# Kernel tuning notes

Hardware: AMD Instinct MI355X
Metric: run time of the kernel (lower is better)

The kernel has to match this reference:

```python
import jax, jax.numpy as jnp
import numpy as np

N_TOK = 2048      # flattened batch*seq tokens
D_MODEL = 1024    # in_features
D_INT = 512       # d_intermediate
N_EXPERTS = 8     # n_routed_experts
TOP_K = 2         # n_activated_experts


def setup_inputs() -> dict:
    key = jax.random.key(0)
    k1, k2, k3, k4, k5 = jax.random.split(key, 5)
    x = jax.random.normal(k1, (N_TOK, D_MODEL), dtype=jnp.float32)
    indices = jax.random.randint(k2, (N_TOK, TOP_K), 0, N_EXPERTS, dtype=jnp.int32)
    # router combine weights (normalized over top-k like a softmax router)
    weights = jax.nn.softmax(jax.random.normal(k3, (N_TOK, TOP_K), dtype=jnp.float32), axis=-1)
    # tokens-per-expert counts, consistent with indices (as the router would supply)
    counts = jnp.bincount(indices.reshape(-1), length=N_EXPERTS).astype(jnp.int32)
    # expert weights: fc1 -> 2*d_int (gated MLP), fc2 -> d_model; kaiming-ish scale
    s1 = 1.0 / np.sqrt(D_MODEL)
    s2 = 1.0 / np.sqrt(D_INT)
    fc1_weight = jax.random.uniform(k4, (N_EXPERTS, 2 * D_INT, D_MODEL), jnp.float32, -s1, s1)
    fc2_weight = jax.random.uniform(k5, (N_EXPERTS, D_MODEL, D_INT), jnp.float32, -s2, s2)
    return {"x": x, "weights": weights, "indices": indices, "counts": counts,
            "fc1_weight": fc1_weight, "fc2_weight": fc2_weight}


def reference(x, weights, indices, counts, fc1_weight, fc2_weight):
    # Dense dispatch-free formulation: run every token through every expert's
    # gated MLP, then gather the per-slot expert output. Identical math to the
    # sort / grouped-GEMM / scatter path for the selected (token, expert) pairs.
    # h: (n_tok, n_experts, 2*d_int)
    h = jnp.einsum('td,egd->teg', x, fc1_weight)
    y, z = jnp.split(h, 2, axis=-1)
    a = y * jax.nn.silu(z)  # GatedMLP: y * activation(z)
    # expert outputs: (n_tok, n_experts, d_model)
    out = jnp.einsum('tei,edi->ted', a, fc2_weight)
    # gather the chosen expert output for each of the top-k slots: (n_tok, k, d_model)
    per_slot = jnp.take_along_axis(out, indices[:, :, None], axis=1)
    # combine: z = bmm(weights[:, None], x_by_expert).squeeze(1)
    return jnp.einsum('tk,tkd->td', weights, per_slot)
```

## Files before the change

kernel.cpp:

```cpp
#include <hip/hip_runtime.h>

typedef unsigned short u16;
typedef unsigned int u32;
using short8  = __attribute__((ext_vector_type(8))) short;
using floatx4 = __attribute__((ext_vector_type(4))) float;

#define N_TOK   2048
#define D_MODEL 1024
#define D_INT   512
#define NE      8

#define O_TOK    0
#define O_WROW   24576
#define O_XG     65536
#define O_ACT    10551296
#define O_FC1B   36765696
#define O_FC2B   53542912

static __device__ inline u16 f2bf(float f) {
    u32 u = __builtin_bit_cast(u32, f);
    u = (u + 0x7fffu + ((u >> 16) & 1u)) >> 16;
    return (u16)u;
}
static __device__ inline u32 pack2(float a, float b) {
    return (u32)f2bf(a) | ((u32)f2bf(b) << 16);
}
static __device__ inline void glds16(const u16* g, u16* l) {
    __builtin_amdgcn_global_load_lds(
        (const __attribute__((address_space(1))) void*)g,
        (__attribute__((address_space(3))) void*)l, 16, 0, 0);
}

__global__ __launch_bounds__(256) void prep_kernel(
    const float* __restrict__ x, const float* __restrict__ wts,
    const int* __restrict__ indices, const int* __restrict__ counts,
    const float* __restrict__ fc1, const float* __restrict__ fc2,
    u16* __restrict__ fc1b, u16* __restrict__ fc2b,
    u16* __restrict__ Xg, int* __restrict__ tok, float* __restrict__ wrow,
    float* __restrict__ out) {
    int b = blockIdx.x, tid = threadIdx.x;
    if (b < 6144) {
        size_t v = (size_t)b * 256 + tid;
        const float* src; u16* dst; size_t off;
        if (v < 1048576) { src = fc1; dst = fc1b; off = v * 8; }
        else             { src = fc2; dst = fc2b; off = (v - 1048576) * 8; }
        const floatx4* s4 = reinterpret_cast<const floatx4*>(src + off);
        floatx4 a = s4[0], bb = s4[1];
        uint4 o;
        o.x = pack2(a[0], a[1]); o.y = pack2(a[2], a[3]);
        o.z = pack2(bb[0], bb[1]); o.w = pack2(bb[2], bb[3]);
        *reinterpret_cast<uint4*>(dst + off) = o;
        return;
    }
    if (b < 8192) {
        int t = b - 6144;
        int off[NE];
        {
            int acc = 0;
            #pragma unroll
            for (int e = 0; e < NE; e++) { off[e] = acc; acc += ((counts[e] + 63) >> 6) << 6; }
        }
        int e0 = indices[2 * t], e1 = indices[2 * t + 1];
        __shared__ int s0, s1;
        if (tid == 0) { s0 = 0; s1 = 0; }
        __syncthreads();
        int c0 = 0, c1 = 0;
        const int4* ip = reinterpret_cast<const int4*>(indices);
        #pragma unroll
        for (int i = 0; i < 4; i++) {
            int4 vv = ip[tid * 4 + i];
            int q = tid * 16 + i * 4;
            c0 += (q + 0 < 2 * t && vv.x == e0) + (q + 1 < 2 * t && vv.y == e0)
                + (q + 2 < 2 * t && vv.z == e0) + (q + 3 < 2 * t && vv.w == e0);
            c1 += (q + 0 <= 2 * t && vv.x == e1) + (q + 1 <= 2 * t && vv.y == e1)
                + (q + 2 <= 2 * t && vv.z == e1) + (q + 3 <= 2 * t && vv.w == e1);
        }
        if (c0) atomicAdd(&s0, c0);
        if (c1) atomicAdd(&s1, c1);
        __syncthreads();
        int r0 = off[e0] + s0;
        int r1 = off[e1] + s1;
        if (tid == 0) {
            tok[r0] = t; tok[r1] = t;
            wrow[r0] = wts[2 * t]; wrow[r1] = wts[2 * t + 1];
        }
        const floatx4* src = reinterpret_cast<const floatx4*>(x + (size_t)t * D_MODEL);
        floatx4 a = src[tid];
        uint2 o;
        o.x = pack2(a[0], a[1]); o.y = pack2(a[2], a[3]);
        *reinterpret_cast<uint2*>(Xg + (size_t)r0 * D_MODEL + tid * 4) = o;
        *reinterpret_cast<uint2*>(Xg + (size_t)r1 * D_MODEL + tid * 4) = o;
        return;
    }
    {
        int z = b - 8192;
        floatx4* dst = reinterpret_cast<floatx4*>(out) + (size_t)z * 1024;
        #pragma unroll
        for (int i = 0; i < 4; i++) dst[i * 256 + tid] = (floatx4){0.f, 0.f, 0.f, 0.f};
        return;
    }
}

__global__ __launch_bounds__(256) void gemm1_kernel(
    const u16* __restrict__ Xg, const u16* __restrict__ fc1b,
    u16* __restrict__ Act, const int* __restrict__ counts) {
    __shared__ u16 As[64 * 64];
    __shared__ u16 Bs[128 * 64];
    int tid = threadIdx.x;
    int soff[NE + 1];
    {
        int acc = 0;
        #pragma unroll
        for (int e2 = 0; e2 < NE; e2++) { soff[e2] = acc; acc += ((counts[e2] + 63) >> 6) << 6; }
        soff[NE] = acc;
    }
    int row0 = blockIdx.y * 64;
    if (row0 >= soff[NE]) return;
    int e = 0;
    while (soff[e + 1] <= row0) e++;
    int bx = blockIdx.x;
    const u16* A  = Xg + (size_t)row0 * 1024;
    const u16* Be = fc1b + (size_t)e * 1024 * 1024;

    int lane = tid & 63, w = tid >> 6;
    int m0 = (w >> 1) * 32, n0 = (w & 1) * 32;
    int lr = lane & 15, kq = lane >> 4;

    const u16* gA[2]; u16* lA[2];
    #pragma unroll
    for (int j = 0; j < 2; j++) {
        int v = tid + j * 256;
        int r = v >> 3, kb = (v & 7) ^ (r & 7);
        gA[j] = A + (size_t)r * 1024 + kb * 8;
        lA[j] = As + (w * 64 + j * 256) * 8;
    }
    const u16* gB[4]; u16* lB[4];
    #pragma unroll
    for (int j = 0; j < 4; j++) {
        int v = tid + j * 256;
        int r = v >> 3, kb = (v & 7) ^ (r & 7);
        int grow = (r < 64) ? (bx * 64 + r) : (448 + bx * 64 + r);
        gB[j] = Be + (size_t)grow * 1024 + kb * 8;
        lB[j] = Bs + (w * 64 + j * 256) * 8;
    }

    floatx4 aY[2][2], aZ[2][2];
    #pragma unroll
    for (int i = 0; i < 2; i++)
        #pragma unroll
        for (int j = 0; j < 2; j++) {
            aY[i][j] = (floatx4){0.f, 0.f, 0.f, 0.f};
            aZ[i][j] = (floatx4){0.f, 0.f, 0.f, 0.f};
        }

    for (int k0 = 0; k0 < 1024; k0 += 64) {
        glds16(gA[0] + k0, lA[0]); glds16(gA[1] + k0, lA[1]);
        glds16(gB[0] + k0, lB[0]); glds16(gB[1] + k0, lB[1]);
        glds16(gB[2] + k0, lB[2]); glds16(gB[3] + k0, lB[3]);
        __syncthreads();
        #pragma unroll
        for (int ks = 0; ks < 2; ks++) {
            int sw = ((ks * 4 + kq) ^ (lr & 7)) * 8;
            short8 af[2], by[2], bz[2];
            #pragma unroll
            for (int i = 0; i < 2; i++)
                af[i] = *reinterpret_cast<const short8*>(&As[(m0 + i * 16 + lr) * 64 + sw]);
            #pragma unroll
            for (int j = 0; j < 2; j++) {
                by[j] = *reinterpret_cast<const short8*>(&Bs[(n0 + j * 16 + lr) * 64 + sw]);
                bz[j] = *reinterpret_cast<const short8*>(&Bs[(64 + n0 + j * 16 + lr) * 64 + sw]);
            }
            #pragma unroll
            for (int i = 0; i < 2; i++)
                #pragma unroll
                for (int j = 0; j < 2; j++) {
                    aY[i][j] = __builtin_amdgcn_mfma_f32_16x16x32_bf16(af[i], by[j], aY[i][j], 0, 0, 0);
                    aZ[i][j] = __builtin_amdgcn_mfma_f32_16x16x32_bf16(af[i], bz[j], aZ[i][j], 0, 0, 0);
                }
        }
        __syncthreads();
    }
    #pragma unroll
    for (int i = 0; i < 2; i++)
        #pragma unroll
        for (int j = 0; j < 2; j++) {
            floatx4 y = aY[i][j], z = aZ[i][j];
            #pragma unroll
            for (int r = 0; r < 4; r++) {
                float zz = z[r];
                float av = y[r] * (zz / (1.0f + __expf(-zz)));
                int m = m0 + i * 16 + kq * 4 + r;
                int g = bx * 64 + n0 + j * 16 + lr;
                Act[(size_t)(row0 + m) * D_INT + g] = f2bf(av);
            }
        }
}

__global__ __launch_bounds__(256) void gemm2_kernel(
    const u16* __restrict__ Act, const u16* __restrict__ fc2b,
    float* __restrict__ out, const int* __restrict__ counts,
    const int* __restrict__ tok, const float* __restrict__ wrow) {
    __shared__ u16 As[64 * 64];
    __shared__ u16 Bs[128 * 64];
    __shared__ int sTok[64];
    __shared__ float sW[64];
    int tid = threadIdx.x;
    int soff[NE + 1];
    {
        int acc = 0;
        #pragma unroll
        for (int e2 = 0; e2 < NE; e2++) { soff[e2] = acc; acc += ((counts[e2] + 63) >> 6) << 6; }
        soff[NE] = acc;
    }
    int row0 = blockIdx.y * 64;
    if (row0 >= soff[NE]) return;
    int e = 0;
    while (soff[e + 1] <= row0) e++;
    int bx = blockIdx.x;
    const u16* A  = Act + (size_t)row0 * 512;
    const u16* Be = fc2b + (size_t)e * 1024 * 512;

    int lane = tid & 63, w = tid >> 6;
    int m0 = (w >> 1) * 32, n0 = (w & 1) * 64;
    int lr = lane & 15, kq = lane >> 4;

    const u16* gA[2]; u16* lA[2];
    #pragma unroll
    for (int j = 0; j < 2; j++) {
        int v = tid + j * 256;
        int r = v >> 3, kb = (v & 7) ^ (r & 7);
        gA[j] = A + (size_t)r * 512 + kb * 8;
        lA[j] = As + (w * 64 + j * 256) * 8;
    }
    const u16* gB[4]; u16* lB[4];
    #pragma unroll
    for (int j = 0; j < 4; j++) {
        int v = tid + j * 256;
        int r = v >> 3, kb = (v & 7) ^ (r & 7);
        gB[j] = Be + (size_t)(bx * 128 + r) * 512 + kb * 8;
        lB[j] = Bs + (w * 64 + j * 256) * 8;
    }

    floatx4 acc[2][4];
    #pragma unroll
    for (int i = 0; i < 2; i++)
        #pragma unroll
        for (int j = 0; j < 4; j++) acc[i][j] = (floatx4){0.f, 0.f, 0.f, 0.f};

    for (int k0 = 0; k0 < 512; k0 += 64) {
        glds16(gA[0] + k0, lA[0]); glds16(gA[1] + k0, lA[1]);
        glds16(gB[0] + k0, lB[0]); glds16(gB[1] + k0, lB[1]);
        glds16(gB[2] + k0, lB[2]); glds16(gB[3] + k0, lB[3]);
        __syncthreads();
        #pragma unroll
        for (int ks = 0; ks < 2; ks++) {
            int sw = ((ks * 4 + kq) ^ (lr & 7)) * 8;
            short8 af[2], bf[4];
            #pragma unroll
            for (int i = 0; i < 2; i++)
                af[i] = *reinterpret_cast<const short8*>(&As[(m0 + i * 16 + lr) * 64 + sw]);
            #pragma unroll
            for (int j = 0; j < 4; j++)
                bf[j] = *reinterpret_cast<const short8*>(&Bs[(n0 + j * 16 + lr) * 64 + sw]);
            #pragma unroll
            for (int i = 0; i < 2; i++)
                #pragma unroll
                for (int j = 0; j < 4; j++)
                    acc[i][j] = __builtin_amdgcn_mfma_f32_16x16x32_bf16(af[i], bf[j], acc[i][j], 0, 0, 0);
        }
        __syncthreads();
    }
    if (tid < 64) {
        int g = row0 + tid;
        bool val = (g - soff[e]) < counts[e];
        sTok[tid] = val ? tok[g] : -1;
        sW[tid]   = val ? wrow[g] : 0.f;
    }
    __syncthreads();
    #pragma unroll
    for (int i = 0; i < 2; i++)
        #pragma unroll
        for (int r = 0; r < 4; r++) {
            int m = m0 + i * 16 + kq * 4 + r;
            int t = sTok[m];
            if (t >= 0) {
                float wgt = sW[m];
                float* dst = out + (size_t)t * D_MODEL + bx * 128;
                #pragma unroll
                for (int j = 0; j < 4; j++)
                    atomicAdd(dst + n0 + j * 16 + lr, wgt * acc[i][j][r]);
            }
        }
}

extern "C" void kernel_launch(void* const* d_in, const int* in_sizes, int n_in,
                              void* d_out, int out_size, void* d_ws, size_t ws_size,
                              hipStream_t stream) {
    const float* x       = (const float*)d_in[0];
    const float* wts     = (const float*)d_in[1];
    const int*   indices = (const int*)d_in[2];
    const int*   counts  = (const int*)d_in[3];
    const float* fc1     = (const float*)d_in[4];
    const float* fc2     = (const float*)d_in[5];
    float* out = (float*)d_out;
    char* ws = (char*)d_ws;

    int*   tok  = (int*)(ws + O_TOK);
    float* wrow = (float*)(ws + O_WROW);
    u16*   Xg   = (u16*)(ws + O_XG);
    u16*   Act  = (u16*)(ws + O_ACT);
    u16*   fc1b = (u16*)(ws + O_FC1B);
    u16*   fc2b = (u16*)(ws + O_FC2B);

    prep_kernel<<<8704, 256, 0, stream>>>(x, wts, indices, counts, fc1, fc2,
                                          fc1b, fc2b, Xg, tok, wrow, out);
    gemm1_kernel<<<dim3(8, 72), 256, 0, stream>>>(Xg, fc1b, Act, counts);
    gemm2_kernel<<<dim3(8, 72), 256, 0, stream>>>(Act, fc2b, out, counts, tok, wrow);
}
```

Measured before the change: 151.6 us.

## Double-buffer LDS tiles in both expert GEMM kernels to overlap loads with MFMA

Both grouped GEMM kernels now keep two LDS buffers for the A and B tiles. The first tile is loaded before the loop, and each iteration issues the direct global-to-LDS loads for the next K tile before running MFMAs on the current one. This aims to hide global load latency behind compute and removes the barrier that followed the loads. In exchange LDS use per block doubles, which may lower occupancy, and correctness depends on the end-of-loop barrier waiting for the outstanding loads.

```diff
diff --git a/kernel.cpp b/kernel.cpp
--- a/kernel.cpp
+++ b/kernel.cpp
@@ -104,8 +104,8 @@
 __global__ __launch_bounds__(256) void gemm1_kernel(
     const u16* __restrict__ Xg, const u16* __restrict__ fc1b,
     u16* __restrict__ Act, const int* __restrict__ counts) {
-    __shared__ u16 As[64 * 64];
-    __shared__ u16 Bs[128 * 64];
+    __shared__ u16 As[2][64 * 64];
+    __shared__ u16 Bs[2][128 * 64];
     int tid = threadIdx.x;
     int soff[NE + 1];
     {
@@ -126,22 +126,22 @@
     int m0 = (w >> 1) * 32, n0 = (w & 1) * 32;
     int lr = lane & 15, kq = lane >> 4;
 
-    const u16* gA[2]; u16* lA[2];
+    const u16* gA[2]; int oA[2];
     #pragma unroll
     for (int j = 0; j < 2; j++) {
         int v = tid + j * 256;
         int r = v >> 3, kb = (v & 7) ^ (r & 7);
         gA[j] = A + (size_t)r * 1024 + kb * 8;
-        lA[j] = As + (w * 64 + j * 256) * 8;
-    }
-    const u16* gB[4]; u16* lB[4];
+        oA[j] = (w * 64 + j * 256) * 8;
+    }
+    const u16* gB[4]; int oB[4];
     #pragma unroll
     for (int j = 0; j < 4; j++) {
         int v = tid + j * 256;
         int r = v >> 3, kb = (v & 7) ^ (r & 7);
         int grow = (r < 64) ? (bx * 64 + r) : (448 + bx * 64 + r);
         gB[j] = Be + (size_t)grow * 1024 + kb * 8;
-        lB[j] = Bs + (w * 64 + j * 256) * 8;
+        oB[j] = (w * 64 + j * 256) * 8;
     }
 
     floatx4 aY[2][2], aZ[2][2];
@@ -153,22 +153,31 @@
             aZ[i][j] = (floatx4){0.f, 0.f, 0.f, 0.f};
         }
 
+    glds16(gA[0], &As[0][oA[0]]); glds16(gA[1], &As[0][oA[1]]);
+    glds16(gB[0], &Bs[0][oB[0]]); glds16(gB[1], &Bs[0][oB[1]]);
+    glds16(gB[2], &Bs[0][oB[2]]); glds16(gB[3], &Bs[0][oB[3]]);
+    __syncthreads();
+
     for (int k0 = 0; k0 < 1024; k0 += 64) {
-        glds16(gA[0] + k0, lA[0]); glds16(gA[1] + k0, lA[1]);
-        glds16(gB[0] + k0, lB[0]); glds16(gB[1] + k0, lB[1]);
-        glds16(gB[2] + k0, lB[2]); glds16(gB[3] + k0, lB[3]);
-        __syncthreads();
+        int buf = (k0 >> 6) & 1;
+        int nk = k0 + 64;
+        if (nk < 1024) {
+            int nb = buf ^ 1;
+            glds16(gA[0] + nk, &As[nb][oA[0]]); glds16(gA[1] + nk, &As[nb][oA[1]]);
+            glds16(gB[0] + nk, &Bs[nb][oB[0]]); glds16(gB[1] + nk, &Bs[nb][oB[1]]);
+            glds16(gB[2] + nk, &Bs[nb][oB[2]]); glds16(gB[3] + nk, &Bs[nb][oB[3]]);
+        }
         #pragma unroll
         for (int ks = 0; ks < 2; ks++) {
             int sw = ((ks * 4 + kq) ^ (lr & 7)) * 8;
             short8 af[2], by[2], bz[2];
             #pragma unroll
             for (int i = 0; i < 2; i++)
-                af[i] = *reinterpret_cast<const short8*>(&As[(m0 + i * 16 + lr) * 64 + sw]);
+                af[i] = *reinterpret_cast<const short8*>(&As[buf][(m0 + i * 16 + lr) * 64 + sw]);
             #pragma unroll
             for (int j = 0; j < 2; j++) {
-                by[j] = *reinterpret_cast<const short8*>(&Bs[(n0 + j * 16 + lr) * 64 + sw]);
-                bz[j] = *reinterpret_cast<const short8*>(&Bs[(64 + n0 + j * 16 + lr) * 64 + sw]);
+                by[j] = *reinterpret_cast<const short8*>(&Bs[buf][(n0 + j * 16 + lr) * 64 + sw]);
+                bz[j] = *reinterpret_cast<const short8*>(&Bs[buf][(64 + n0 + j * 16 + lr) * 64 + sw]);
             }
             #pragma unroll
             for (int i = 0; i < 2; i++)
@@ -200,8 +209,8 @@
     const u16* __restrict__ Act, const u16* __restrict__ fc2b,
     float* __restrict__ out, const int* __restrict__ counts,
     const int* __restrict__ tok, const float* __restrict__ wrow) {
-    __shared__ u16 As[64 * 64];
-    __shared__ u16 Bs[128 * 64];
+    __shared__ u16 As[2][64 * 64];
+    __shared__ u16 Bs[2][128 * 64];
     __shared__ int sTok[64];
     __shared__ float sW[64];
     int tid = threadIdx.x;
@@ -224,21 +233,21 @@
     int m0 = (w >> 1) * 32, n0 = (w & 1) * 64;
     int lr = lane & 15, kq = lane >> 4;
 
-    const u16* gA[2]; u16* lA[2];
+    const u16* gA[2]; int oA[2];
     #pragma unroll
     for (int j = 0; j < 2; j++) {
         int v = tid + j * 256;
         int r = v >> 3, kb = (v & 7) ^ (r & 7);
         gA[j] = A + (size_t)r * 512 + kb * 8;
-        lA[j] = As + (w * 64 + j * 256) * 8;
-    }
-    const u16* gB[4]; u16* lB[4];
+        oA[j] = (w * 64 + j * 256) * 8;
+    }
+    const u16* gB[4]; int oB[4];
     #pragma unroll
     for (int j = 0; j < 4; j++) {
         int v = tid + j * 256;
         int r = v >> 3, kb = (v & 7) ^ (r & 7);
         gB[j] = Be + (size_t)(bx * 128 + r) * 512 + kb * 8;
-        lB[j] = Bs + (w * 64 + j * 256) * 8;
+        oB[j] = (w * 64 + j * 256) * 8;
     }
 
     floatx4 acc[2][4];
@@ -247,21 +256,30 @@
         #pragma unroll
         for (int j = 0; j < 4; j++) acc[i][j] = (floatx4){0.f, 0.f, 0.f, 0.f};
 
+    glds16(gA[0], &As[0][oA[0]]); glds16(gA[1], &As[0][oA[1]]);
+    glds16(gB[0], &Bs[0][oB[0]]); glds16(gB[1], &Bs[0][oB[1]]);
+    glds16(gB[2], &Bs[0][oB[2]]); glds16(gB[3], &Bs[0][oB[3]]);
+    __syncthreads();
+
     for (int k0 = 0; k0 < 512; k0 += 64) {
-        glds16(gA[0] + k0, lA[0]); glds16(gA[1] + k0, lA[1]);
-        glds16(gB[0] + k0, lB[0]); glds16(gB[1] + k0, lB[1]);
-        glds16(gB[2] + k0, lB[2]); glds16(gB[3] + k0, lB[3]);
-        __syncthreads();
+        int buf = (k0 >> 6) & 1;
+        int nk = k0 + 64;
+        if (nk < 512) {
+            int nb = buf ^ 1;
+            glds16(gA[0] + nk, &As[nb][oA[0]]); glds16(gA[1] + nk, &As[nb][oA[1]]);
+            glds16(gB[0] + nk, &Bs[nb][oB[0]]); glds16(gB[1] + nk, &Bs[nb][oB[1]]);
+            glds16(gB[2] + nk, &Bs[nb][oB[2]]); glds16(gB[3] + nk, &Bs[nb][oB[3]]);
+        }
         #pragma unroll
         for (int ks = 0; ks < 2; ks++) {
             int sw = ((ks * 4 + kq) ^ (lr & 7)) * 8;
             short8 af[2], bf[4];
             #pragma unroll
             for (int i = 0; i < 2; i++)
-                af[i] = *reinterpret_cast<const short8*>(&As[(m0 + i * 16 + lr) * 64 + sw]);
+                af[i] = *reinterpret_cast<const short8*>(&As[buf][(m0 + i * 16 + lr) * 64 + sw]);
             #pragma unroll
             for (int j = 0; j < 4; j++)
-                bf[j] = *reinterpret_cast<const short8*>(&Bs[(n0 + j * 16 + lr) * 64 + sw]);
+                bf[j] = *reinterpret_cast<const short8*>(&Bs[buf][(n0 + j * 16 + lr) * 64 + sw]);
             #pragma unroll
             for (int i = 0; i < 2; i++)
                 #pragma unroll
```

New measurement: 153.7 us. No clear change (+1.4%).

## Fuse fp32-to-bf16 conversion and token gather into the grouped GEMM loads

Applied to the files above, without the earlier changes.

Drops the prep pass that converted all expert weights and gathered x rows into bf16 workspace buffers. The GEMMs now read fp32 x (gathered via the token table) and fp32 fc1/fc2 directly, convert to bf16 in registers and store into LDS. The routing kernel shrinks to computing the token/weight tables and zeroing the output. This removes a large standalone read/write pass over the weights. In exchange each GEMM block reads twice the bytes per tile, repeats the conversion across row blocks, and gives up the direct global-to-LDS loads for those operands.

```diff
diff --git a/kernel.cpp b/kernel.cpp
--- a/kernel.cpp
+++ b/kernel.cpp
@@ -11,11 +11,8 @@
 #define NE      8
 
 #define O_TOK    0
-#define O_WROW   24576
-#define O_XG     65536
-#define O_ACT    10551296
-#define O_FC1B   36765696
-#define O_FC2B   53542912
+#define O_WROW   32768
+#define O_ACT    65536
 
 static __device__ inline u16 f2bf(float f) {
     u32 u = __builtin_bit_cast(u32, f);
@@ -25,85 +22,67 @@
 static __device__ inline u32 pack2(float a, float b) {
     return (u32)f2bf(a) | ((u32)f2bf(b) << 16);
 }
+static __device__ inline uint4 pack8(floatx4 a, floatx4 b) {
+    uint4 o;
+    o.x = pack2(a[0], a[1]); o.y = pack2(a[2], a[3]);
+    o.z = pack2(b[0], b[1]); o.w = pack2(b[2], b[3]);
+    return o;
+}
 static __device__ inline void glds16(const u16* g, u16* l) {
     __builtin_amdgcn_global_load_lds(
         (const __attribute__((address_space(1))) void*)g,
         (__attribute__((address_space(3))) void*)l, 16, 0, 0);
 }
 
-__global__ __launch_bounds__(256) void prep_kernel(
-    const float* __restrict__ x, const float* __restrict__ wts,
-    const int* __restrict__ indices, const int* __restrict__ counts,
-    const float* __restrict__ fc1, const float* __restrict__ fc2,
-    u16* __restrict__ fc1b, u16* __restrict__ fc2b,
-    u16* __restrict__ Xg, int* __restrict__ tok, float* __restrict__ wrow,
-    float* __restrict__ out) {
+__global__ __launch_bounds__(256) void route_kernel(
+    const float* __restrict__ wts, const int* __restrict__ indices,
+    const int* __restrict__ counts,
+    int* __restrict__ tok, float* __restrict__ wrow, float* __restrict__ out) {
     int b = blockIdx.x, tid = threadIdx.x;
-    if (b < 6144) {
-        size_t v = (size_t)b * 256 + tid;
-        const float* src; u16* dst; size_t off;
-        if (v < 1048576) { src = fc1; dst = fc1b; off = v * 8; }
-        else             { src = fc2; dst = fc2b; off = (v - 1048576) * 8; }
-        const floatx4* s4 = reinterpret_cast<const floatx4*>(src + off);
-        floatx4 a = s4[0], bb = s4[1];
-        uint4 o;
-        o.x = pack2(a[0], a[1]); o.y = pack2(a[2], a[3]);
-        o.z = pack2(bb[0], bb[1]); o.w = pack2(bb[2], bb[3]);
-        *reinterpret_cast<uint4*>(dst + off) = o;
+    if (b >= 2048) {
+        int z = b - 2048;
+        floatx4* dst = reinterpret_cast<floatx4*>(out) + (size_t)z * 1024;
+        #pragma unroll
+        for (int i = 0; i < 4; i++) dst[i * 256 + tid] = (floatx4){0.f, 0.f, 0.f, 0.f};
         return;
     }
-    if (b < 8192) {
-        int t = b - 6144;
-        int off[NE];
-        {
-            int acc = 0;
-            #pragma unroll
-            for (int e = 0; e < NE; e++) { off[e] = acc; acc += ((counts[e] + 63) >> 6) << 6; }
-        }
-        int e0 = indices[2 * t], e1 = indices[2 * t + 1];
-        __shared__ int s0, s1;
-        if (tid == 0) { s0 = 0; s1 = 0; }
-        __syncthreads();
-        int c0 = 0, c1 = 0;
-        const int4* ip = reinterpret_cast<const int4*>(indices);
-        #pragma unroll
-        for (int i = 0; i < 4; i++) {
-            int4 vv = ip[tid * 4 + i];
-            int q = tid * 16 + i * 4;
-            c0 += (q + 0 < 2 * t && vv.x == e0) + (q + 1 < 2 * t && vv.y == e0)
-                + (q + 2 < 2 * t && vv.z == e0) + (q + 3 < 2 * t && vv.w == e0);
-            c1 += (q + 0 <= 2 * t && vv.x == e1) + (q + 1 <= 2 * t && vv.y == e1)
-                + (q + 2 <= 2 * t && vv.z == e1) + (q + 3 <= 2 * t && vv.w == e1);
-        }
-        if (c0) atomicAdd(&s0, c0);
-        if (c1) atomicAdd(&s1, c1);
-        __syncthreads();
+    int t = b;
+    int off[NE];
+    {
+        int acc = 0;
+        #pragma unroll
+        for (int e = 0; e < NE; e++) { off[e] = acc; acc += ((counts[e] + 63) >> 6) << 6; }
+    }
+    int e0 = indices[2 * t], e1 = indices[2 * t + 1];
+    __shared__ int s0, s1;
+    if (tid == 0) { s0 = 0; s1 = 0; }
+    __syncthreads();
+    int c0 = 0, c1 = 0;
+    const int4* ip = reinterpret_cast<const int4*>(indices);
+    #pragma unroll
+    for (int i = 0; i < 4; i++) {
+        int4 vv = ip[tid * 4 + i];
+        int q = tid * 16 + i * 4;
+        c0 += (q + 0 < 2 * t && vv.x == e0) + (q + 1 < 2 * t && vv.y == e0)
+            + (q + 2 < 2 * t && vv.z == e0) + (q + 3 < 2 * t && vv.w == e0);
+        c1 += (q + 0 <= 2 * t && vv.x == e1) + (q + 1 <= 2 * t && vv.y == e1)
+            + (q + 2 <= 2 * t && vv.z == e1) + (q + 3 <= 2 * t && vv.w == e1);
+    }
+    if (c0) atomicAdd(&s0, c0);
+    if (c1) atomicAdd(&s1, c1);
+    __syncthreads();
+    if (tid == 0) {
         int r0 = off[e0] + s0;
         int r1 = off[e1] + s1;
-        if (tid == 0) {
-            tok[r0] = t; tok[r1] = t;
-            wrow[r0] = wts[2 * t]; wrow[r1] = wts[2 * t + 1];
-        }
-        const floatx4* src = reinterpret_cast<const floatx4*>(x + (size_t)t * D_MODEL);
-        floatx4 a = src[tid];
-        uint2 o;
-        o.x = pack2(a[0], a[1]); o.y = pack2(a[2], a[3]);
-        *reinterpret_cast<uint2*>(Xg + (size_t)r0 * D_MODEL + tid * 4) = o;
-        *reinterpret_cast<uint2*>(Xg + (size_t)r1 * D_MODEL + tid * 4) = o;
-        return;
-    }
-    {
-        int z = b - 8192;
-        floatx4* dst = reinterpret_cast<floatx4*>(out) + (size_t)z * 1024;
-        #pragma unroll
-        for (int i = 0; i < 4; i++) dst[i * 256 + tid] = (floatx4){0.f, 0.f, 0.f, 0.f};
-        return;
+        tok[r0] = t; tok[r1] = t;
+        wrow[r0] = wts[2 * t]; wrow[r1] = wts[2 * t + 1];
     }
 }
 
 __global__ __launch_bounds__(256) void gemm1_kernel(
-    const u16* __restrict__ Xg, const u16* __restrict__ fc1b,
-    u16* __restrict__ Act, const int* __restrict__ counts) {
+    const float* __restrict__ x, const float* __restrict__ fc1,
+    u16* __restrict__ Act, const int* __restrict__ counts,
+    const int* __restrict__ tok) {
     __shared__ u16 As[64 * 64];
     __shared__ u16 Bs[128 * 64];
     int tid = threadIdx.x;
@@ -118,30 +97,27 @@
     if (row0 >= soff[NE]) return;
     int e = 0;
     while (soff[e + 1] <= row0) e++;
+    int cnte = counts[e];
     int bx = blockIdx.x;
-    const u16* A  = Xg + (size_t)row0 * 1024;
-    const u16* Be = fc1b + (size_t)e * 1024 * 1024;
+    const float* Be = fc1 + (size_t)e * 1024 * 1024;
 
     int lane = tid & 63, w = tid >> 6;
     int m0 = (w >> 1) * 32, n0 = (w & 1) * 32;
     int lr = lane & 15, kq = lane >> 4;
 
-    const u16* gA[2]; u16* lA[2];
-    #pragma unroll
-    for (int j = 0; j < 2; j++) {
-        int v = tid + j * 256;
-        int r = v >> 3, kb = (v & 7) ^ (r & 7);
-        gA[j] = A + (size_t)r * 1024 + kb * 8;
-        lA[j] = As + (w * 64 + j * 256) * 8;
-    }
-    const u16* gB[4]; u16* lB[4];
+    int rA0 = tid >> 3, rA1 = rA0 + 32;
+    int kbA0 = (tid & 7) ^ (rA0 & 7), kbA1 = (tid & 7) ^ (rA1 & 7);
+    int tA0 = (row0 + rA0 - soff[e]) < cnte ? tok[row0 + rA0] : 0;
+    int tA1 = (row0 + rA1 - soff[e]) < cnte ? tok[row0 + rA1] : 0;
+    const float* gA0 = x + (size_t)tA0 * 1024 + kbA0 * 8;
+    const float* gA1 = x + (size_t)tA1 * 1024 + kbA1 * 8;
+    const float* gB[4];
     #pragma unroll
     for (int j = 0; j < 4; j++) {
         int v = tid + j * 256;
         int r = v >> 3, kb = (v & 7) ^ (r & 7);
         int grow = (r < 64) ? (bx * 64 + r) : (448 + bx * 64 + r);
         gB[j] = Be + (size_t)grow * 1024 + kb * 8;
-        lB[j] = Bs + (w * 64 + j * 256) * 8;
     }
 
     floatx4 aY[2][2], aZ[2][2];
@@ -154,9 +130,22 @@
         }
 
     for (int k0 = 0; k0 < 1024; k0 += 64) {
-        glds16(gA[0] + k0, lA[0]); glds16(gA[1] + k0, lA[1]);
-        glds16(gB[0] + k0, lB[0]); glds16(gB[1] + k0, lB[1]);
-        glds16(gB[2] + k0, lB[2]); glds16(gB[3] + k0, lB[3]);
+        floatx4 a0l = *reinterpret_cast<const floatx4*>(gA0 + k0);
+        floatx4 a0h = *reinterpret_cast<const floatx4*>(gA0 + k0 + 4);
+        floatx4 a1l = *reinterpret_cast<const floatx4*>(gA1 + k0);
+        floatx4 a1h = *reinterpret_cast<const floatx4*>(gA1 + k0 + 4);
+        floatx4 bl[4], bh[4];
+        #pragma unroll
+        for (int j = 0; j < 4; j++) {
+            bl[j] = *reinterpret_cast<const floatx4*>(gB[j] + k0);
+            bh[j] = *reinterpret_cast<const floatx4*>(gB[j] + k0 + 4);
+        }
+        __syncthreads();
+        *reinterpret_cast<uint4*>(&As[(size_t)tid * 8])         = pack8(a0l, a0h);
+        *reinterpret_cast<uint4*>(&As[(size_t)(tid + 256) * 8]) = pack8(a1l, a1h);
+        #pragma unroll
+        for (int j = 0; j < 4; j++)
+            *reinterpret_cast<uint4*>(&Bs[(size_t)(tid + j * 256) * 8]) = pack8(bl[j], bh[j]);
         __syncthreads();
         #pragma unroll
         for (int ks = 0; ks < 2; ks++) {
@@ -178,7 +167,6 @@
                     aZ[i][j] = __builtin_amdgcn_mfma_f32_16x16x32_bf16(af[i], bz[j], aZ[i][j], 0, 0, 0);
                 }
         }
-        __syncthreads();
     }
     #pragma unroll
     for (int i = 0; i < 2; i++)
@@ -197,7 +185,7 @@
 }
 
 __global__ __launch_bounds__(256) void gemm2_kernel(
-    const u16* __restrict__ Act, const u16* __restrict__ fc2b,
+    const u16* __restrict__ Act, const float* __restrict__ fc2,
     float* __restrict__ out, const int* __restrict__ counts,
     const int* __restrict__ tok, const float* __restrict__ wrow) {
     __shared__ u16 As[64 * 64];
@@ -218,27 +206,26 @@
     while (soff[e + 1] <= row0) e++;
     int bx = blockIdx.x;
     const u16* A  = Act + (size_t)row0 * 512;
-    const u16* Be = fc2b + (size_t)e * 1024 * 512;
+    const float* Be = fc2 + (size_t)e * 1024 * 512;
 
     int lane = tid & 63, w = tid >> 6;
     int m0 = (w >> 1) * 32, n0 = (w & 1) * 64;
     int lr = lane & 15, kq = lane >> 4;
 
-    const u16* gA[2]; u16* lA[2];
+    const u16* gA[2]; int oA[2];
     #pragma unroll
     for (int j = 0; j < 2; j++) {
         int v = tid + j * 256;
         int r = v >> 3, kb = (v & 7) ^ (r & 7);
         gA[j] = A + (size_t)r * 512 + kb * 8;
-        lA[j] = As + (w * 64 + j * 256) * 8;
-    }
-    const u16* gB[4]; u16* lB[4];
+        oA[j] = (w * 64 + j * 256) * 8;
+    }
+    const float* gB[4];
     #pragma unroll
     for (int j = 0; j < 4; j++) {
         int v = tid + j * 256;
         int r = v >> 3, kb = (v & 7) ^ (r & 7);
         gB[j] = Be + (size_t)(bx * 128 + r) * 512 + kb * 8;
-        lB[j] = Bs + (w * 64 + j * 256) * 8;
     }
 
     floatx4 acc[2][4];
@@ -248,9 +235,18 @@
         for (int j = 0; j < 4; j++) acc[i][j] = (floatx4){0.f, 0.f, 0.f, 0.f};
 
     for (int k0 = 0; k0 < 512; k0 += 64) {
-        glds16(gA[0] + k0, lA[0]); glds16(gA[1] + k0, lA[1]);
-        glds16(gB[0] + k0, lB[0]); glds16(gB[1] + k0, lB[1]);
-        glds16(gB[2] + k0, lB[2]); glds16(gB[3] + k0, lB[3]);
+        floatx4 bl[4], bh[4];
+        #pragma unroll
+        for (int j = 0; j < 4; j++) {
+            bl[j] = *reinterpret_cast<const floatx4*>(gB[j] + k0);
+            bh[j] = *reinterpret_cast<const floatx4*>(gB[j] + k0 + 4);
+        }
+        __syncthreads();
+        glds16(gA[0] + k0, &As[oA[0]]);
+        glds16(gA[1] + k0, &As[oA[1]]);
+        #pragma unroll
+        for (int j = 0; j < 4; j++)
+            *reinterpret_cast<uint4*>(&Bs[(size_t)(tid + j * 256) * 8]) = pack8(bl[j], bh[j]);
         __syncthreads();
         #pragma unroll
         for (int ks = 0; ks < 2; ks++) {
@@ -268,7 +264,6 @@
                 for (int j = 0; j < 4; j++)
                     acc[i][j] = __builtin_amdgcn_mfma_f32_16x16x32_bf16(af[i], bf[j], acc[i][j], 0, 0, 0);
         }
-        __syncthreads();
     }
     if (tid < 64) {
         int g = row0 + tid;
@@ -307,13 +302,9 @@
 
     int*   tok  = (int*)(ws + O_TOK);
     float* wrow = (float*)(ws + O_WROW);
-    u16*   Xg   = (u16*)(ws + O_XG);
     u16*   Act  = (u16*)(ws + O_ACT);
-    u16*   fc1b = (u16*)(ws + O_FC1B);
-    u16*   fc2b = (u16*)(ws + O_FC2B);
-
-    prep_kernel<<<8704, 256, 0, stream>>>(x, wts, indices, counts, fc1, fc2,
-                                          fc1b, fc2b, Xg, tok, wrow, out);
-    gemm1_kernel<<<dim3(8, 72), 256, 0, stream>>>(Xg, fc1b, Act, counts);
-    gemm2_kernel<<<dim3(8, 72), 256, 0, stream>>>(Act, fc2b, out, counts, tok, wrow);
-}
+
+    route_kernel<<<2560, 256, 0, stream>>>(wts, indices, counts, tok, wrow, out);
+    gemm1_kernel<<<dim3(8, 72), 256, 0, stream>>>(x, fc1, Act, counts, tok);
+    gemm2_kernel<<<dim3(8, 72), 256, 0, stream>>>(Act, fc2, out, counts, tok, wrow);
+}
```

Measured after the change: 164.5 us. 1.09x slower.

## Fuse prep and both expert GEMMs into one persistent cooperative kernel

Applied to the files above, without the earlier changes.

Merges the prep, gemm1 and gemm2 launches into a single persistent cooperative kernel of 512 blocks. Each block loops over the former block indices, and grid-wide syncs separate the three phases. This removes two kernel-launch gaps and the tail idle time between kernels. In exchange it adds grid barrier cost and limits parallelism to 512 resident blocks, so the prep phase with 8704 work items runs serially in strided loops.

```diff
diff --git a/kernel.cpp b/kernel.cpp
--- a/kernel.cpp
+++ b/kernel.cpp
@@ -1,4 +1,7 @@
 #include <hip/hip_runtime.h>
+#include <hip/hip_cooperative_groups.h>
+
+namespace cg = cooperative_groups;
 
 typedef unsigned short u16;
 typedef unsigned int u32;
@@ -31,266 +34,256 @@
         (__attribute__((address_space(3))) void*)l, 16, 0, 0);
 }
 
-__global__ __launch_bounds__(256) void prep_kernel(
+__global__ __launch_bounds__(256, 4) void moe_kernel(
     const float* __restrict__ x, const float* __restrict__ wts,
     const int* __restrict__ indices, const int* __restrict__ counts,
     const float* __restrict__ fc1, const float* __restrict__ fc2,
     u16* __restrict__ fc1b, u16* __restrict__ fc2b,
-    u16* __restrict__ Xg, int* __restrict__ tok, float* __restrict__ wrow,
+    u16* __restrict__ Xg, u16* __restrict__ Act,
+    int* __restrict__ tok, float* __restrict__ wrow,
     float* __restrict__ out) {
-    int b = blockIdx.x, tid = threadIdx.x;
-    if (b < 6144) {
-        size_t v = (size_t)b * 256 + tid;
-        const float* src; u16* dst; size_t off;
-        if (v < 1048576) { src = fc1; dst = fc1b; off = v * 8; }
-        else             { src = fc2; dst = fc2b; off = (v - 1048576) * 8; }
-        const floatx4* s4 = reinterpret_cast<const floatx4*>(src + off);
-        floatx4 a = s4[0], bb = s4[1];
-        uint4 o;
-        o.x = pack2(a[0], a[1]); o.y = pack2(a[2], a[3]);
-        o.z = pack2(bb[0], bb[1]); o.w = pack2(bb[2], bb[3]);
-        *reinterpret_cast<uint4*>(dst + off) = o;
-        return;
-    }
-    if (b < 8192) {
-        int t = b - 6144;
-        int off[NE];
-        {
-            int acc = 0;
-            #pragma unroll
-            for (int e = 0; e < NE; e++) { off[e] = acc; acc += ((counts[e] + 63) >> 6) << 6; }
-        }
-        int e0 = indices[2 * t], e1 = indices[2 * t + 1];
-        __shared__ int s0, s1;
-        if (tid == 0) { s0 = 0; s1 = 0; }
-        __syncthreads();
-        int c0 = 0, c1 = 0;
-        const int4* ip = reinterpret_cast<const int4*>(indices);
-        #pragma unroll
-        for (int i = 0; i < 4; i++) {
-            int4 vv = ip[tid * 4 + i];
-            int q = tid * 16 + i * 4;
-            c0 += (q + 0 < 2 * t && vv.x == e0) + (q + 1 < 2 * t && vv.y == e0)
-                + (q + 2 < 2 * t && vv.z == e0) + (q + 3 < 2 * t && vv.w == e0);
-            c1 += (q + 0 <= 2 * t && vv.x == e1) + (q + 1 <= 2 * t && vv.y == e1)
-                + (q + 2 <= 2 * t && vv.z == e1) + (q + 3 <= 2 * t && vv.w == e1);
-        }
-        if (c0) atomicAdd(&s0, c0);
-        if (c1) atomicAdd(&s1, c1);
-        __syncthreads();
-        int r0 = off[e0] + s0;
-        int r1 = off[e1] + s1;
-        if (tid == 0) {
-            tok[r0] = t; tok[r1] = t;
-            wrow[r0] = wts[2 * t]; wrow[r1] = wts[2 * t + 1];
-        }
-        const floatx4* src = reinterpret_cast<const floatx4*>(x + (size_t)t * D_MODEL);
-        floatx4 a = src[tid];
-        uint2 o;
-        o.x = pack2(a[0], a[1]); o.y = pack2(a[2], a[3]);
-        *reinterpret_cast<uint2*>(Xg + (size_t)r0 * D_MODEL + tid * 4) = o;
-        *reinterpret_cast<uint2*>(Xg + (size_t)r1 * D_MODEL + tid * 4) = o;
-        return;
-    }
-    {
-        int z = b - 8192;
-        floatx4* dst = reinterpret_cast<floatx4*>(out) + (size_t)z * 1024;
-        #pragma unroll
-        for (int i = 0; i < 4; i++) dst[i * 256 + tid] = (floatx4){0.f, 0.f, 0.f, 0.f};
-        return;
-    }
-}
-
-__global__ __launch_bounds__(256) void gemm1_kernel(
-    const u16* __restrict__ Xg, const u16* __restrict__ fc1b,
-    u16* __restrict__ Act, const int* __restrict__ counts) {
     __shared__ u16 As[64 * 64];
     __shared__ u16 Bs[128 * 64];
-    int tid = threadIdx.x;
+    __shared__ int sTok[64];
+    __shared__ float sW[64];
+    __shared__ int sCnt[2];
+
+    const int b = blockIdx.x, tid = threadIdx.x;
+    cg::grid_group grid = cg::this_grid();
+
     int soff[NE + 1];
     {
         int acc = 0;
         #pragma unroll
-        for (int e2 = 0; e2 < NE; e2++) { soff[e2] = acc; acc += ((counts[e2] + 63) >> 6) << 6; }
+        for (int e = 0; e < NE; e++) { soff[e] = acc; acc += ((counts[e] + 63) >> 6) << 6; }
         soff[NE] = acc;
     }
-    int row0 = blockIdx.y * 64;
-    if (row0 >= soff[NE]) return;
-    int e = 0;
-    while (soff[e + 1] <= row0) e++;
-    int bx = blockIdx.x;
-    const u16* A  = Xg + (size_t)row0 * 1024;
-    const u16* Be = fc1b + (size_t)e * 1024 * 1024;
-
-    int lane = tid & 63, w = tid >> 6;
-    int m0 = (w >> 1) * 32, n0 = (w & 1) * 32;
-    int lr = lane & 15, kq = lane >> 4;
-
-    const u16* gA[2]; u16* lA[2];
-    #pragma unroll
-    for (int j = 0; j < 2; j++) {
-        int v = tid + j * 256;
-        int r = v >> 3, kb = (v & 7) ^ (r & 7);
-        gA[j] = A + (size_t)r * 1024 + kb * 8;
-        lA[j] = As + (w * 64 + j * 256) * 8;
+    const int nT = (soff[NE] >> 6) * 8;
+
+    const int lane = tid & 63, w = tid >> 6;
+    const int lr = lane & 15, kq = lane >> 4;
+
+    #pragma unroll 1
+    for (int i = 0; i < 17; i++) {
+        int j = i * 512 + b;
+        if (j < 6144) {
+            size_t v = (size_t)j * 256 + tid;
+            const float* src; u16* dst; size_t off;
+            if (v < 1048576) { src = fc1; dst = fc1b; off = v * 8; }
+            else             { src = fc2; dst = fc2b; off = (v - 1048576) * 8; }
+            const floatx4* s4 = reinterpret_cast<const floatx4*>(src + off);
+            floatx4 a = s4[0], bb = s4[1];
+            uint4 o;
+            o.x = pack2(a[0], a[1]); o.y = pack2(a[2], a[3]);
+            o.z = pack2(bb[0], bb[1]); o.w = pack2(bb[2], bb[3]);
+            *reinterpret_cast<uint4*>(dst + off) = o;
+        } else if (j < 8192) {
+            int t = j - 6144;
+            int e0 = indices[2 * t], e1 = indices[2 * t + 1];
+            if (tid == 0) { sCnt[0] = 0; sCnt[1] = 0; }
+            __syncthreads();
+            int c0 = 0, c1 = 0;
+            const int4* ip = reinterpret_cast<const int4*>(indices);
+            #pragma unroll
+            for (int q4 = 0; q4 < 4; q4++) {
+                int4 vv = ip[tid * 4 + q4];
+                int q = tid * 16 + q4 * 4;
+                c0 += (q + 0 < 2 * t && vv.x == e0) + (q + 1 < 2 * t && vv.y == e0)
+                    + (q + 2 < 2 * t && vv.z == e0) + (q + 3 < 2 * t && vv.w == e0);
+                c1 += (q + 0 <= 2 * t && vv.x == e1) + (q + 1 <= 2 * t && vv.y == e1)
+                    + (q + 2 <= 2 * t && vv.z == e1) + (q + 3 <= 2 * t && vv.w == e1);
+            }
+            if (c0) atomicAdd(&sCnt[0], c0);
+            if (c1) atomicAdd(&sCnt[1], c1);
+            __syncthreads();
+            int r0 = soff[e0] + sCnt[0];
+            int r1 = soff[e1] + sCnt[1];
+            if (tid == 0) {
+                tok[r0] = t; tok[r1] = t;
+                wrow[r0] = wts[2 * t]; wrow[r1] = wts[2 * t + 1];
+            }
+            const floatx4* src = reinterpret_cast<const floatx4*>(x + (size_t)t * D_MODEL);
+            floatx4 a = src[tid];
+            uint2 o;
+            o.x = pack2(a[0], a[1]); o.y = pack2(a[2], a[3]);
+            *reinterpret_cast<uint2*>(Xg + (size_t)r0 * D_MODEL + tid * 4) = o;
+            *reinterpret_cast<uint2*>(Xg + (size_t)r1 * D_MODEL + tid * 4) = o;
+            __syncthreads();
+        } else {
+            int z = j - 8192;
+            floatx4* dst = reinterpret_cast<floatx4*>(out) + (size_t)z * 1024;
+            #pragma unroll
+            for (int q = 0; q < 4; q++) dst[q * 256 + tid] = (floatx4){0.f, 0.f, 0.f, 0.f};
+        }
     }
-    const u16* gB[4]; u16* lB[4];
-    #pragma unroll
-    for (int j = 0; j < 4; j++) {
-        int v = tid + j * 256;
-        int r = v >> 3, kb = (v & 7) ^ (r & 7);
-        int grow = (r < 64) ? (bx * 64 + r) : (448 + bx * 64 + r);
-        gB[j] = Be + (size_t)grow * 1024 + kb * 8;
-        lB[j] = Bs + (w * 64 + j * 256) * 8;
+    __threadfence();
+    grid.sync();
+
+    {
+        const int m0 = (w >> 1) * 32, n0 = (w & 1) * 32;
+        #pragma unroll 1
+        for (int T = b; T < nT; T += 512) {
+            int bx = T & 7, row0 = (T >> 3) * 64;
+            int e = 0;
+            while (soff[e + 1] <= row0) e++;
+            const u16* A  = Xg + (size_t)row0 * 1024;
+            const u16* Be = fc1b + (size_t)e * 1024 * 1024;
+
+            const u16* gA[2]; u16* lA[2];
+            #pragma unroll
+            for (int p = 0; p < 2; p++) {
+                int v = tid + p * 256;
+                int r = v >> 3, kb = (v & 7) ^ (r & 7);
+                gA[p] = A + (size_t)r * 1024 + kb * 8;
+                lA[p] = As + (size_t)(w * 64 + p * 256) * 8;
+            }
+            const u16* gB[4]; u16* lB[4];
+            #pragma unroll
+            for (int p = 0; p < 4; p++) {
+                int v = tid + p * 256;
+                int r = v >> 3, kb = (v & 7) ^ (r & 7);
+                int grow = (r < 64) ? (bx * 64 + r) : (448 + bx * 64 + r);
+                gB[p] = Be + (size_t)grow * 1024 + kb * 8;
+                lB[p] = Bs + (size_t)(w * 64 + p * 256) * 8;
+            }
+
+            floatx4 aY[2][2], aZ[2][2];
+            #pragma unroll
+            for (int i = 0; i < 2; i++)
+                #pragma unroll
+                for (int j = 0; j < 2; j++) {
+                    aY[i][j] = (floatx4){0.f, 0.f, 0.f, 0.f};
+                    aZ[i][j] = (floatx4){0.f, 0.f, 0.f, 0.f};
+                }
+
+            #pragma unroll 1
+            for (int k0 = 0; k0 < 1024; k0 += 64) {
+                glds16(gA[0] + k0, lA[0]); glds16(gA[1] + k0, lA[1]);
+                glds16(gB[0] + k0, lB[0]); glds16(gB[1] + k0, lB[1]);
+                glds16(gB[2] + k0, lB[2]); glds16(gB[3] + k0, lB[3]);
+                __syncthreads();
+                #pragma unroll
+                for (int ks = 0; ks < 2; ks++) {
+                    int sw = ((ks * 4 + kq) ^ (lr & 7)) * 8;
+                    short8 af[2], by[2], bz[2];
+                    #pragma unroll
+                    for (int i = 0; i < 2; i++)
+                        af[i] = *reinterpret_cast<const short8*>(&As[(m0 + i * 16 + lr) * 64 + sw]);
+                    #pragma unroll
+                    for (int j = 0; j < 2; j++) {
+                        by[j] = *reinterpret_cast<const short8*>(&Bs[(n0 + j * 16 + lr) * 64 + sw]);
+                        bz[j] = *reinterpret_cast<const short8*>(&Bs[(64 + n0 + j * 16 + lr) * 64 + sw]);
+                    }
+                    #pragma unroll
+                    for (int i = 0; i < 2; i++)
+                        #pragma unroll
+                        for (int j = 0; j < 2; j++) {
+                            aY[i][j] = __builtin_amdgcn_mfma_f32_16x16x32_bf16(af[i], by[j], aY[i][j], 0, 0, 0);
+                            aZ[i][j] = __builtin_amdgcn_mfma_f32_16x16x32_bf16(af[i], bz[j], aZ[i][j], 0, 0, 0);
+                        }
+                }
+                __syncthreads();
+            }
+            #pragma unroll
+            for (int i = 0; i < 2; i++)
+                #pragma unroll
+                for (int j = 0; j < 2; j++) {
+                    floatx4 y = aY[i][j], z = aZ[i][j];
+                    #pragma unroll
+                    for (int r = 0; r < 4; r++) {
+                        float zz = z[r];
+                        float av = y[r] * (zz / (1.0f + __expf(-zz)));
+                        int m = m0 + i * 16 + kq * 4 + r;
+                        int g = bx * 64 + n0 + j * 16 + lr;
+                        Act[(size_t)(row0 + m) * D_INT + g] = f2bf(av);
+                    }
+                }
+        }
     }
-
-    floatx4 aY[2][2], aZ[2][2];
-    #pragma unroll
-    for (int i = 0; i < 2; i++)
-        #pragma unroll
-        for (int j = 0; j < 2; j++) {
-            aY[i][j] = (floatx4){0.f, 0.f, 0.f, 0.f};
-            aZ[i][j] = (floatx4){0.f, 0.f, 0.f, 0.f};
+    __threadfence();
+    grid.sync();
+
+    {
+        const int m0 = (w >> 1) * 32, n0 = (w & 1) * 64;
+        #pragma unroll 1
+        for (int T = b; T < nT; T += 512) {
+            int bx = T & 7, row0 = (T >> 3) * 64;
+            int e = 0;
+            while (soff[e + 1] <= row0) e++;
+            const u16* A  = Act + (size_t)row0 * 512;
+            const u16* Be = fc2b + (size_t)e * 1024 * 512;
+
+            const u16* gA[2]; u16* lA[2];
+            #pragma unroll
+            for (int p = 0; p < 2; p++) {
+                int v = tid + p * 256;
+                int r = v >> 3, kb = (v & 7) ^ (r & 7);
+                gA[p] = A + (size_t)r * 512 + kb * 8;
+                lA[p] = As + (size_t)(w * 64 + p * 256) * 8;
+            }
+            const u16* gB[4]; u16* lB[4];
+            #pragma unroll
+            for (int p = 0; p < 4; p++) {
+                int v = tid + p * 256;
+                int r = v >> 3, kb = (v & 7) ^ (r & 7);
+                gB[p] = Be + (size_t)(bx * 128 + r) * 512 + kb * 8;
+                lB[p] = Bs + (size_t)(w * 64 + p * 256) * 8;
+            }
+
+            floatx4 acc[2][4];
+            #pragma unroll
+            for (int i = 0; i < 2; i++)
+                #pragma unroll
+                for (int j = 0; j < 4; j++) acc[i][j] = (floatx4){0.f, 0.f, 0.f, 0.f};
+
+            #pragma unroll 1
+            for (int k0 = 0; k0 < 512; k0 += 64) {
+                glds16(gA[0] + k0, lA[0]); glds16(gA[1] + k0, lA[1]);
+                glds16(gB[0] + k0, lB[0]); glds16(gB[1] + k0, lB[1]);
+                glds16(gB[2] + k0, lB[2]); glds16(gB[3] + k0, lB[3]);
+                __syncthreads();
+                #pragma unroll
+                for (int ks = 0; ks < 2; ks++) {
+                    int sw = ((ks * 4 + kq) ^ (lr & 7)) * 8;
+                    short8 af[2], bf[4];
+                    #pragma unroll
+                    for (int i = 0; i < 2; i++)
+                        af[i] = *reinterpret_cast<const short8*>(&As[(m0 + i * 16 + lr) * 64 + sw]);
+                    #pragma unroll
+                    for (int j = 0; j < 4; j++)
+                        bf[j] = *reinterpret_cast<const short8*>(&Bs[(n0 + j * 16 + lr) * 64 + sw]);
+                    #pragma unroll
+                    for (int i = 0; i < 2; i++)
+                        #pragma unroll
+                        for (int j = 0; j < 4; j++)
+                            acc[i][j] = __builtin_amdgcn_mfma_f32_16x16x32_bf16(af[i], bf[j], acc[i][j], 0, 0, 0);
+                }
+                __syncthreads();
+            }
+            if (tid < 64) {
+                int g = row0 + tid;
+                bool val = (g - soff[e]) < counts[e];
+                sTok[tid] = val ? tok[g] : -1;
+                sW[tid]   = val ? wrow[g] : 0.f;
+            }
+            __syncthreads();
+            #pragma unroll
+            for (int i = 0; i < 2; i++)
+                #pragma unroll
+                for (int r = 0; r < 4; r++) {
+                    int m = m0 + i * 16 + kq * 4 + r;
+                    int t = sTok[m];
+                    if (t >= 0) {
+                        float wgt = sW[m];
+                        float* dst = out + (size_t)t * D_MODEL + bx * 128;
+                        #pragma unroll
+                        for (int j = 0; j < 4; j++)
+                            atomicAdd(dst + n0 + j * 16 + lr, wgt * acc[i][j][r]);
+                    }
+                }
+            __syncthreads();
         }
-
-    for (int k0 = 0; k0 < 1024; k0 += 64) {
-        glds16(gA[0] + k0, lA[0]); glds16(gA[1] + k0, lA[1]);
-        glds16(gB[0] + k0, lB[0]); glds16(gB[1] + k0, lB[1]);
-        glds16(gB[2] + k0, lB[2]); glds16(gB[3] + k0, lB[3]);
-        __syncthreads();
-        #pragma unroll
-        for (int ks = 0; ks < 2; ks++) {
-            int sw = ((ks * 4 + kq) ^ (lr & 7)) * 8;
-            short8 af[2], by[2], bz[2];
-            #pragma unroll
-            for (int i = 0; i < 2; i++)
-                af[i] = *reinterpret_cast<const short8*>(&As[(m0 + i * 16 + lr) * 64 + sw]);
-            #pragma unroll
-            for (int j = 0; j < 2; j++) {
-                by[j] = *reinterpret_cast<const short8*>(&Bs[(n0 + j * 16 + lr) * 64 + sw]);
-                bz[j] = *reinterpret_cast<const short8*>(&Bs[(64 + n0 + j * 16 + lr) * 64 + sw]);
-            }
-            #pragma unroll
-            for (int i = 0; i < 2; i++)
-                #pragma unroll
-                for (int j = 0; j < 2; j++) {
-                    aY[i][j] = __builtin_amdgcn_mfma_f32_16x16x32_bf16(af[i], by[j], aY[i][j], 0, 0, 0);
-                    aZ[i][j] = __builtin_amdgcn_mfma_f32_16x16x32_bf16(af[i], bz[j], aZ[i][j], 0, 0, 0);
-                }
-        }
-        __syncthreads();
     }
-    #pragma unroll
-    for (int i = 0; i < 2; i++)
-        #pragma unroll
-        for (int j = 0; j < 2; j++) {
-            floatx4 y = aY[i][j], z = aZ[i][j];
-            #pragma unroll
-            for (int r = 0; r < 4; r++) {
-                float zz = z[r];
-                float av = y[r] * (zz / (1.0f + __expf(-zz)));
-                int m = m0 + i * 16 + kq * 4 + r;
-                int g = bx * 64 + n0 + j * 16 + lr;
-                Act[(size_t)(row0 + m) * D_INT + g] = f2bf(av);
-            }
-        }
-}
-
-__global__ __launch_bounds__(256) void gemm2_kernel(
-    const u16* __restrict__ Act, const u16* __restrict__ fc2b,
-    float* __restrict__ out, const int* __restrict__ counts,
-    const int* __restrict__ tok, const float* __restrict__ wrow) {
-    __shared__ u16 As[64 * 64];
-    __shared__ u16 Bs[128 * 64];
-    __shared__ int sTok[64];
-    __shared__ float sW[64];
-    int tid = threadIdx.x;
-    int soff[NE + 1];
-    {
-        int acc = 0;
-        #pragma unroll
-        for (int e2 = 0; e2 < NE; e2++) { soff[e2] = acc; acc += ((counts[e2] + 63) >> 6) << 6; }
-        soff[NE] = acc;
-    }
-    int row0 = blockIdx.y * 64;
-    if (row0 >= soff[NE]) return;
-    int e = 0;
-    while (soff[e + 1] <= row0) e++;
-    int bx = blockIdx.x;
-    const u16* A  = Act + (size_t)row0 * 512;
-    const u16* Be = fc2b + (size_t)e * 1024 * 512;
-
-    int lane = tid & 63, w = tid >> 6;
-    int m0 = (w >> 1) * 32, n0 = (w & 1) * 64;
-    int lr = lane & 15, kq = lane >> 4;
-
-    const u16* gA[2]; u16* lA[2];
-    #pragma unroll
-    for (int j = 0; j < 2; j++) {
-        int v = tid + j * 256;
-        int r = v >> 3, kb = (v & 7) ^ (r & 7);
-        gA[j] = A + (size_t)r * 512 + kb * 8;
-        lA[j] = As + (w * 64 + j * 256) * 8;
-    }
-    const u16* gB[4]; u16* lB[4];
-    #pragma unroll
-    for (int j = 0; j < 4; j++) {
-        int v = tid + j * 256;
-        int r = v >> 3, kb = (v & 7) ^ (r & 7);
-        gB[j] = Be + (size_t)(bx * 128 + r) * 512 + kb * 8;
-        lB[j] = Bs + (w * 64 + j * 256) * 8;
-    }
-
-    floatx4 acc[2][4];
-    #pragma unroll
-    for (int i = 0; i < 2; i++)
-        #pragma unroll
-        for (int j = 0; j < 4; j++) acc[i][j] = (floatx4){0.f, 0.f, 0.f, 0.f};
-
-    for (int k0 = 0; k0 < 512; k0 += 64) {
-        glds16(gA[0] + k0, lA[0]); glds16(gA[1] + k0, lA[1]);
-        glds16(gB[0] + k0, lB[0]); glds16(gB[1] + k0, lB[1]);
-        glds16(gB[2] + k0, lB[2]); glds16(gB[3] + k0, lB[3]);
-        __syncthreads();
-        #pragma unroll
-        for (int ks = 0; ks < 2; ks++) {
-            int sw = ((ks * 4 + kq) ^ (lr & 7)) * 8;
-            short8 af[2], bf[4];
-            #pragma unroll
-            for (int i = 0; i < 2; i++)
-                af[i] = *reinterpret_cast<const short8*>(&As[(m0 + i * 16 + lr) * 64 + sw]);
-            #pragma unroll
-            for (int j = 0; j < 4; j++)
-                bf[j] = *reinterpret_cast<const short8*>(&Bs[(n0 + j * 16 + lr) * 64 + sw]);
-            #pragma unroll
-            for (int i = 0; i < 2; i++)
-                #pragma unroll
-                for (int j = 0; j < 4; j++)
-                    acc[i][j] = __builtin_amdgcn_mfma_f32_16x16x32_bf16(af[i], bf[j], acc[i][j], 0, 0, 0);
-        }
-        __syncthreads();
-    }
-    if (tid < 64) {
-        int g = row0 + tid;
-        bool val = (g - soff[e]) < counts[e];
-        sTok[tid] = val ? tok[g] : -1;
-        sW[tid]   = val ? wrow[g] : 0.f;
-    }
-    __syncthreads();
-    #pragma unroll
-    for (int i = 0; i < 2; i++)
-        #pragma unroll
-        for (int r = 0; r < 4; r++) {
-            int m = m0 + i * 16 + kq * 4 + r;
-            int t = sTok[m];
-            if (t >= 0) {
-                float wgt = sW[m];
-                float* dst = out + (size_t)t * D_MODEL + bx * 128;
-                #pragma unroll
-                for (int j = 0; j < 4; j++)
-                    atomicAdd(dst + n0 + j * 16 + lr, wgt * acc[i][j][r]);
-            }
-        }
 }
 
 extern "C" void kernel_launch(void* const* d_in, const int* in_sizes, int n_in,
@@ -312,8 +305,8 @@
     u16*   fc1b = (u16*)(ws + O_FC1B);
     u16*   fc2b = (u16*)(ws + O_FC2B);
 
-    prep_kernel<<<8704, 256, 0, stream>>>(x, wts, indices, counts, fc1, fc2,
-                                          fc1b, fc2b, Xg, tok, wrow, out);
-    gemm1_kernel<<<dim3(8, 72), 256, 0, stream>>>(Xg, fc1b, Act, counts);
-    gemm2_kernel<<<dim3(8, 72), 256, 0, stream>>>(Act, fc2b, out, counts, tok, wrow);
-}
+    void* args[] = {&x, &wts, &indices, &counts, &fc1, &fc2,
+                    &fc1b, &fc2b, &Xg, &Act, &tok, &wrow, &out};
+    hipLaunchCooperativeKernel((const void*)moe_kernel, dim3(512), dim3(256),
+                               args, 0, stream);
+}
```

New measurement: 403.7 us. 166% more time.
